# Kernel optimization log

Measured on AMD Instinct MI355X. Metric: run time of the kernel, lower is better.

## Reference

```python
import jax, jax.numpy as jnp
import numpy as np

B, C, R, E, H = 32, 64, 63, 256, 4
D = E // H  # head dim = 64


def setup_inputs() -> dict:
    key = jax.random.key(0)
    ks = jax.random.split(key, 8)
    s = 0.02
    return {
        "x": jax.random.normal(ks[0], (B, C, R, E), jnp.float32),
        "real_cols": jax.random.randint(ks[1], (B,), 0, C),
        "cls_token": jax.random.normal(ks[2], (E,), jnp.float32),
        "w_in": (jax.random.normal(ks[3], (3 * E, E), jnp.float32) * s),
        "b_in": jnp.zeros((3 * E,), jnp.float32),
        "w_out": (jax.random.normal(ks[4], (E, E), jnp.float32) * s),
        "b_out": jnp.zeros((E,), jnp.float32),
        "ln_g": jnp.ones((E,), jnp.float32),
        "ln_b": jnp.zeros((E,), jnp.float32),
        "w1": (jax.random.normal(ks[5], (E, E), jnp.float32) * s),
        "b1": jnp.zeros((E,), jnp.float32),
        "w2": (jax.random.normal(ks[6], (E, E), jnp.float32) * s),
        "b2": jnp.zeros((E,), jnp.float32),
    }


def reference(x, real_cols, cls_token, w_in, b_in, w_out, b_out, ln_g, ln_b, w1, b1, w2, b2):
    # x: (B, C, R, E); one fused batched MHA+LN+FFN over all (B, C) columns.
    Bq, Cq, Rq, Eq = x.shape
    S = Rq + 1
    cls = jnp.broadcast_to(cls_token, (Bq, Cq, 1, Eq))
    seq = jnp.concatenate([cls, x], axis=2)  # (B,C,S,E)

    # torch MultiheadAttention in-projection: x @ W^T + b, packed q|k|v
    qkv = seq @ w_in.T + b_in  # (B,C,S,3E)
    q, k, v = jnp.split(qkv, 3, axis=-1)
    q = q.reshape(Bq, Cq, S, H, D)
    k = k.reshape(Bq, Cq, S, H, D)
    v = v.reshape(Bq, Cq, S, H, D)

    scale = 1.0 / jnp.sqrt(jnp.asarray(D, x.dtype))
    scores = jnp.einsum('bcqhd,bckhd->bchqk', q, k) * scale  # (B,C,H,S,S)
    attn = jax.nn.softmax(scores, axis=-1)
    ctx = jnp.einsum('bchqk,bckhd->bcqhd', attn, v).reshape(Bq, Cq, S, Eq)
    attn_out = ctx @ w_out.T + b_out  # (B,C,S,E)

    # LayerNorm (biased variance, eps=1e-5 as in torch)
    mu = attn_out.mean(axis=-1, keepdims=True)
    var = ((attn_out - mu) ** 2).mean(axis=-1, keepdims=True)
    ln = (attn_out - mu) / jnp.sqrt(var + 1e-5) * ln_g + ln_b

    ffn = jax.nn.relu(ln @ w1.T + b1) @ w2.T + b2
    out = ln + ffn  # (B,C,S,E)

    rep = out[:, :, 0, :]  # rep_mode == 'cls'

    # columns >= real_cols[b] are zero-padded, matching the original loop
    mask = jnp.arange(Cq)[None, :] < real_cols[:, None]
    return jnp.where(mask[..., None], rep, jnp.zeros((), x.dtype))
```

## Files before the change

### kernel.cpp

```cpp
#include <hip/hip_runtime.h>
#include <hip/hip_bf16.h>
#include <cstdint>

typedef unsigned short u16;
typedef uint32_t u32;

#define Bq 32
#define Cq 64
#define Rq 63
#define NB 4

__device__ __forceinline__ float bflo(u32 u){ return __uint_as_float(u << 16); }
__device__ __forceinline__ float bfhi(u32 u){ return __uint_as_float(u & 0xffff0000u); }
__device__ __forceinline__ float bf1(u16 u){ return __uint_as_float(((u32)u) << 16); }
__device__ __forceinline__ u16 tobf(float f){ __hip_bfloat16 h = __float2bfloat16(f); return *(u16*)&h; }

__device__ __forceinline__ bool dtype_is_bf16(const void* ln_g){
    return *(const u32*)ln_g == 0x3F803F80u;
}
__device__ __forceinline__ float ldin(const void* p, int i, bool bf){
    return bf ? bf1(((const u16*)p)[i]) : ((const float*)p)[i];
}


__global__ __launch_bounds__(256) void prep_kernel(
    const void* __restrict__ cls, const void* __restrict__ w_in,
    const void* __restrict__ b_in, const void* __restrict__ w_out,
    const void* __restrict__ w1, const void* __restrict__ w2,
    const void* __restrict__ ln_g_flag,
    float* __restrict__ uf, float* __restrict__ sbf,
    u16* __restrict__ wvT, u16* __restrict__ woT,
    u16* __restrict__ w1T, u16* __restrict__ w2T)
{
    const bool bf = dtype_is_bf16(ln_g_flag);
    const int tid = threadIdx.x;
    const int blk = blockIdx.x;
    __shared__ float q0[256];
    __shared__ __align__(16) float clsf[256];

    if (blk < 256) {
        const int e = blk, j = tid;
        const int dsti = ((j >> 3) * 256 + e) * 8 + (j & 7);
        wvT[dsti] = tobf(ldin(w_in, (512 + e) * 256 + j, bf));
        woT[dsti] = tobf(ldin(w_out, e * 256 + j, bf));
        w1T[dsti] = tobf(ldin(w1,    e * 256 + j, bf));
        w2T[dsti] = tobf(ldin(w2,    e * 256 + j, bf));
        return;
    }

    const int h = blk - 256;
    clsf[tid] = ldin(cls, tid, bf);
    __syncthreads();

    {
        float acc = ldin(b_in, tid, bf);
        if (bf) {
            const u16* wr = (const u16*)w_in + tid * 256;
            #pragma unroll 8
            for (int j8 = 0; j8 < 32; ++j8) {
                uint4 w = *(const uint4*)(wr + j8 * 8);
                const float* c = &clsf[j8 * 8];
                acc += bflo(w.x) * c[0] + bfhi(w.x) * c[1]
                     + bflo(w.y) * c[2] + bfhi(w.y) * c[3]
                     + bflo(w.z) * c[4] + bfhi(w.z) * c[5]
                     + bflo(w.w) * c[6] + bfhi(w.w) * c[7];
            }
        } else {
            const float4* wr = (const float4*)((const float*)w_in + tid * 256);
            #pragma unroll 8
            for (int j4 = 0; j4 < 64; ++j4) {
                float4 w = wr[j4];
                float4 c = *(const float4*)&clsf[j4 * 4];
                acc += w.x * c.x + w.y * c.y + w.z * c.z + w.w * c.w;
            }
        }
        q0[tid] = acc;
    }
    __syncthreads();

    {
        float ua = 0.f;
        #pragma unroll 8
        for (int d = 0; d < 64; ++d)
            ua += q0[h * 64 + d] * ldin(w_in, (256 + h * 64 + d) * 256 + tid, bf);
        uf[h * 256 + tid] = ua * 0.125f;
    }
    if (tid < 64) {
        float p = q0[h * 64 + tid] * ldin(b_in, 256 + h * 64 + tid, bf);
        #pragma unroll
        for (int off = 32; off; off >>= 1) p += __shfl_xor(p, off);
        if (tid == 0) sbf[h] = p * 0.125f;
    }
}

template<int NBv>
__device__ __forceinline__ void dotN(const u16* __restrict__ wp,
                                     const float* __restrict__ vecs, int vstride,
                                     float* __restrict__ acc)
{
    #pragma unroll 2
    for (int j8 = 0; j8 < 32; ++j8) {
        uint4 w = *(const uint4*)(wp + j8 * 2048);
        float w0 = bflo(w.x), w1_ = bfhi(w.x), w2_ = bflo(w.y), w3 = bfhi(w.y);
        float w4 = bflo(w.z), w5 = bfhi(w.z), w6 = bflo(w.w), w7 = bfhi(w.w);
        #pragma unroll
        for (int i = 0; i < NBv; ++i) {
            const float* v = vecs + i * vstride + j8 * 8;
            float4 a = *(const float4*)v;
            float4 bq = *(const float4*)(v + 4);
            acc[i] += w0 * a.x + w1_ * a.y + w2_ * a.z + w3 * a.w
                    + w4 * bq.x + w5 * bq.y + w6 * bq.z + w7 * bq.w;
        }
    }
}

__global__ __launch_bounds__(256) void fused_kernel(
    const void* __restrict__ x, const int* __restrict__ real_cols,
    const void* __restrict__ cls,
    const void* __restrict__ b_in, const void* __restrict__ b_out,
    const void* __restrict__ ln_g, const void* __restrict__ ln_b,
    const void* __restrict__ b1p, const void* __restrict__ b2p,
    const float* __restrict__ uf, const float* __restrict__ sbf,
    const u16* __restrict__ wvT, const u16* __restrict__ woT,
    const u16* __restrict__ w1T, const u16* __restrict__ w2T,
    void* __restrict__ out)
{
    const bool bf = dtype_is_bf16(ln_g);
    const int tid = threadIdx.x;
    const int b = blockIdx.x >> 4;
    const int g = blockIdx.x & 15;
    const int c0 = g * NB;
    const int rc = real_cols[b];
    const int e = tid;

    if (c0 >= rc) {
        #pragma unroll
        for (int i = 0; i < NB; ++i) {
            size_t oi = (((size_t)b << 6) + c0 + i) * 256 + e;
            if (bf) ((u16*)out)[oi] = 0; else ((float*)out)[oi] = 0.f;
        }
        return;
    }

    __shared__ __align__(16) u16   lds_seq[64 * 260];
    __shared__ __align__(16) float lds_u[1024];
    __shared__ __align__(16) float lds_a[256];
    __shared__ float lds_sb[4];
    __shared__ __align__(16) float lds_s[NB * 1024];
    __shared__ __align__(16) float lds_ctx[NB * 256];
    __shared__ __align__(16) float lds_ln[NB * 256];
    __shared__ __align__(16) float lds_h1[NB * 256];
    __shared__ float lds_redA[4 * NB];
    __shared__ float lds_redB[4 * NB];

    #pragma unroll
    for (int q = 0; q < 4; ++q) lds_u[q * 256 + tid] = uf[q * 256 + tid];
    if (tid < 4) lds_sb[tid] = sbf[tid];

    if (bf) {
        if (tid < 32) {
            uint4 val = *(const uint4*)((const u16*)cls + tid * 8);
            uint2* p = (uint2*)&lds_seq[tid * 8];
            p[0] = make_uint2(val.x, val.y);
            p[1] = make_uint2(val.z, val.w);
        }
    } else {
        if (tid < 64) {
            float4 v = *(const float4*)((const float*)cls + tid * 4);
            u32 lo = ((u32)tobf(v.y) << 16) | tobf(v.x);
            u32 hi = ((u32)tobf(v.w) << 16) | tobf(v.z);
            *(uint2*)&lds_seq[tid * 4] = make_uint2(lo, hi);
        }
    }

    const int hw = tid >> 6, lt = tid & 63;

    for (int i = 0; i < NB; ++i) {
        const int c = c0 + i;
        const int bc = (b << 6) + c;
        const bool act = (c < rc);

        if (act) {
            if (bf) {
                const u16* xr = (const u16*)x + (size_t)bc * (Rq * 256);
                #pragma unroll
                for (int k = 0; k < 8; ++k) {
                    int idx = k * 256 + tid;
                    if (idx < 2016) {
                        uint4 val = *(const uint4*)(xr + idx * 8);
                        int tt = (idx >> 5) + 1;
                        int col = (idx & 31) * 8;
                        uint2* p = (uint2*)&lds_seq[tt * 260 + col];
                        p[0] = make_uint2(val.x, val.y);
                        p[1] = make_uint2(val.z, val.w);
                    }
                }
            } else {
                const float* xr = (const float*)x + (size_t)bc * (Rq * 256);
                #pragma unroll
                for (int k = 0; k < 16; ++k) {
                    int idx = k * 256 + tid;
                    if (idx < 4032) {
                        float4 v = *(const float4*)(xr + idx * 4);
                        int tt = (idx >> 6) + 1;
                        int col = (idx & 63) * 4;
                        u32 lo = ((u32)tobf(v.y) << 16) | tobf(v.x);
                        u32 hi = ((u32)tobf(v.w) << 16) | tobf(v.z);
                        *(uint2*)&lds_seq[tt * 260 + col] = make_uint2(lo, hi);
                    }
                }
            }
        }
        __syncthreads();

        if (act) {
            float sc = lds_sb[hw];
            {
                const u16* srow = &lds_seq[lt * 260];
                const float* uh = &lds_u[hw * 256];
                #pragma unroll 8
                for (int j = 0; j < 256; j += 4) {
                    uint2 pv = *(const uint2*)&srow[j];
                    float4 uv = *(const float4*)&uh[j];
                    sc += bflo(pv.x) * uv.x + bfhi(pv.x) * uv.y
                        + bflo(pv.y) * uv.z + bfhi(pv.y) * uv.w;
                }
            }
            float m = sc;
            #pragma unroll
            for (int off = 32; off; off >>= 1) m = fmaxf(m, __shfl_xor(m, off));
            float ev = __expf(sc - m);
            float sum = ev;
            #pragma unroll
            for (int off = 32; off; off >>= 1) sum += __shfl_xor(sum, off);
            lds_a[lt * 4 + hw] = ev / sum;
        }
        __syncthreads();

        {
            float* sp = &lds_s[i * 1024];
            if (act) {
                float s0 = 0.f, s1 = 0.f, s2 = 0.f, s3 = 0.f;
                #pragma unroll 4
                for (int tt = 0; tt < 64; ++tt) {
                    float v = bf1(lds_seq[tt * 260 + tid]);
                    float4 at = *(const float4*)&lds_a[tt * 4];
                    s0 += at.x * v; s1 += at.y * v; s2 += at.z * v; s3 += at.w * v;
                }
                sp[tid]       = s0;
                sp[256 + tid] = s1;
                sp[512 + tid] = s2;
                sp[768 + tid] = s3;
            } else {
                sp[tid] = 0.f; sp[256 + tid] = 0.f;
                sp[512 + tid] = 0.f; sp[768 + tid] = 0.f;
            }
        }
        __syncthreads();
    }

    const int h = tid >> 6;

    {
        float acc[NB];
        float bv = ldin(b_in, 512 + e, bf);
        #pragma unroll
        for (int i = 0; i < NB; ++i) acc[i] = bv;
        dotN<NB>(wvT + e * 8, &lds_s[h * 256], 1024, acc);
        #pragma unroll
        for (int i = 0; i < NB; ++i) lds_ctx[i * 256 + e] = acc[i];
    }
    __syncthreads();

    float ao[NB];
    {
        float bo = ldin(b_out, e, bf);
        #pragma unroll
        for (int i = 0; i < NB; ++i) ao[i] = bo;
        dotN<NB>(woT + e * 8, lds_ctx, 256, ao);
    }

    const int lane = tid & 63, wv = tid >> 6;
    float mu[NB];
    {
        float r[NB];
        #pragma unroll
        for (int i = 0; i < NB; ++i) r[i] = ao[i];
        #pragma unroll
        for (int off = 32; off; off >>= 1) {
            #pragma unroll
            for (int i = 0; i < NB; ++i) r[i] += __shfl_xor(r[i], off);
        }
        if (lane == 0) {
            #pragma unroll
            for (int i = 0; i < NB; ++i) lds_redA[wv * NB + i] = r[i];
        }
    }
    __syncthreads();
    #pragma unroll
    for (int i = 0; i < NB; ++i)
        mu[i] = (lds_redA[i] + lds_redA[NB + i] + lds_redA[2 * NB + i] + lds_redA[3 * NB + i]) * (1.f / 256.f);

    float lnv[NB];
    {
        float r[NB];
        #pragma unroll
        for (int i = 0; i < NB; ++i) { float d = ao[i] - mu[i]; r[i] = d * d; }
        #pragma unroll
        for (int off = 32; off; off >>= 1) {
            #pragma unroll
            for (int i = 0; i < NB; ++i) r[i] += __shfl_xor(r[i], off);
        }
        if (lane == 0) {
            #pragma unroll
            for (int i = 0; i < NB; ++i) lds_redB[wv * NB + i] = r[i];
        }
    }
    __syncthreads();
    {
        float gg = ldin(ln_g, e, bf), bb = ldin(ln_b, e, bf);
        #pragma unroll
        for (int i = 0; i < NB; ++i) {
            float var = (lds_redB[i] + lds_redB[NB + i] + lds_redB[2 * NB + i] + lds_redB[3 * NB + i]) * (1.f / 256.f);
            lnv[i] = (ao[i] - mu[i]) * rsqrtf(var + 1e-5f) * gg + bb;
            lds_ln[i * 256 + e] = lnv[i];
        }
    }
    __syncthreads();

    {
        float h1[NB];
        float bv = ldin(b1p, e, bf);
        #pragma unroll
        for (int i = 0; i < NB; ++i) h1[i] = bv;
        dotN<NB>(w1T + e * 8, lds_ln, 256, h1);
        #pragma unroll
        for (int i = 0; i < NB; ++i) lds_h1[i * 256 + e] = fmaxf(h1[i], 0.f);
    }
    __syncthreads();

    {
        float o[NB];
        float bv = ldin(b2p, e, bf);
        #pragma unroll
        for (int i = 0; i < NB; ++i) o[i] = lnv[i] + bv;
        dotN<NB>(w2T + e * 8, lds_h1, 256, o);
        #pragma unroll
        for (int i = 0; i < NB; ++i) {
            int c = c0 + i;
            float val = (c < rc) ? o[i] : 0.f;
            size_t oi = (((size_t)b << 6) + c) * 256 + e;
            if (bf) ((u16*)out)[oi] = tobf(val); else ((float*)out)[oi] = val;
        }
    }
}

extern "C" void kernel_launch(void* const* d_in, const int* in_sizes, int n_in,
                              void* d_out, int out_size, void* d_ws, size_t ws_size,
                              hipStream_t stream) {
    const void* x     = d_in[0];
    const int* rcols  = (const int*)d_in[1];
    const void* cls   = d_in[2];
    const void* w_in  = d_in[3];
    const void* b_in  = d_in[4];
    const void* w_out = d_in[5];
    const void* b_out = d_in[6];
    const void* ln_g  = d_in[7];
    const void* ln_b  = d_in[8];
    const void* w1    = d_in[9];
    const void* b1    = d_in[10];
    const void* w2    = d_in[11];
    const void* b2    = d_in[12];

    char* ws = (char*)d_ws;
    float* uf  = (float*)(ws);
    float* sbf = (float*)(ws + 4096);
    u16* wvT = (u16*)(ws + 4608);
    u16* woT = (u16*)(ws + 4608 + 131072);
    u16* w1T = (u16*)(ws + 4608 + 2 * 131072);
    u16* w2T = (u16*)(ws + 4608 + 3 * 131072);

    prep_kernel<<<260, 256, 0, stream>>>(cls, w_in, b_in, w_out, w1, w2, ln_g,
                                         uf, sbf, wvT, woT, w1T, w2T);
    fused_kernel<<<Bq * (Cq / NB), 256, 0, stream>>>(x, rcols, cls,
                                                     b_in, b_out, ln_g, ln_b,
                                                     b1, b2, uf, sbf,
                                                     wvT, woT, w1T, w2T, d_out);
}
```

Baseline: 260.2 us.

## Use MFMA bf16 matrix cores for per-column projection layers and prefetch next column

Replaces the scalar fp32 dot-product loops for the V, output, and FFN projections with 16x16x32 bf16 MFMA instructions. The prep kernel lays weights out in MFMA-fragment order, and the intermediate activations are stored as bf16 in a single reused shared buffer. It also prefetches the next column's input into registers while the current column's attention runs. The cost is extra rounding to bf16 of intermediate activations, and only 4 of the 16 MFMA rows carry real data.

```diff
diff --git a/kernel.cpp b/kernel.cpp
--- a/kernel.cpp
+++ b/kernel.cpp
@@ -9,6 +9,10 @@
 #define Cq 64
 #define Rq 63
 #define NB 4
+#define SEQ_ST 264
+
+typedef __attribute__((ext_vector_type(8))) short bf16x8;
+typedef __attribute__((ext_vector_type(4))) float f32x4;
 
 __device__ __forceinline__ float bflo(u32 u){ return __uint_as_float(u << 16); }
 __device__ __forceinline__ float bfhi(u32 u){ return __uint_as_float(u & 0xffff0000u); }
@@ -40,7 +44,7 @@
 
     if (blk < 256) {
         const int e = blk, j = tid;
-        const int dsti = ((j >> 3) * 256 + e) * 8 + (j & 7);
+        const int dsti = (((e >> 4) * 512) + ((j >> 5) * 64) + (((j >> 3) & 3) * 16) + (e & 15)) * 8 + (j & 7);
         wvT[dsti] = tobf(ldin(w_in, (512 + e) * 256 + j, bf));
         woT[dsti] = tobf(ldin(w_out, e * 256 + j, bf));
         w1T[dsti] = tobf(ldin(w1,    e * 256 + j, bf));
@@ -93,23 +97,23 @@
     }
 }
 
-template<int NBv>
-__device__ __forceinline__ void dotN(const u16* __restrict__ wp,
-                                     const float* __restrict__ vecs, int vstride,
-                                     float* __restrict__ acc)
+__device__ __forceinline__ void mfma_layer4(const u16* __restrict__ wbase,
+                                            const u16* __restrict__ Abase,
+                                            int lane, int w,
+                                            f32x4 acc[4])
 {
-    #pragma unroll 2
-    for (int j8 = 0; j8 < 32; ++j8) {
-        uint4 w = *(const uint4*)(wp + j8 * 2048);
-        float w0 = bflo(w.x), w1_ = bfhi(w.x), w2_ = bflo(w.y), w3 = bfhi(w.y);
-        float w4 = bflo(w.z), w5 = bfhi(w.z), w6 = bflo(w.w), w7 = bfhi(w.w);
-        #pragma unroll
-        for (int i = 0; i < NBv; ++i) {
-            const float* v = vecs + i * vstride + j8 * 8;
-            float4 a = *(const float4*)v;
-            float4 bq = *(const float4*)(v + 4);
-            acc[i] += w0 * a.x + w1_ * a.y + w2_ * a.z + w3 * a.w
-                    + w4 * bq.x + w5 * bq.y + w6 * bq.z + w7 * bq.w;
+    bf16x8 af[8];
+    const u16* ap = Abase + (lane & 15) * SEQ_ST + (lane >> 4) * 8;
+    #pragma unroll
+    for (int ks = 0; ks < 8; ++ks)
+        af[ks] = *(const bf16x8*)(ap + ks * 32);
+    const u16* wp0 = wbase + (((w * 4) * 512 + lane) << 3);
+    #pragma unroll
+    for (int ks = 0; ks < 8; ++ks) {
+        #pragma unroll
+        for (int nt = 0; nt < 4; ++nt) {
+            bf16x8 bfr = *(const bf16x8*)(wp0 + ((nt * 512 + ks * 64) << 3));
+            acc[nt] = __builtin_amdgcn_mfma_f32_16x16x32_bf16(af[ks], bfr, acc[nt], 0, 0, 0);
         }
     }
 }
@@ -142,16 +146,18 @@
         return;
     }
 
-    __shared__ __align__(16) u16   lds_seq[64 * 260];
-    __shared__ __align__(16) float lds_u[1024];
-    __shared__ __align__(16) float lds_a[256];
-    __shared__ float lds_sb[4];
-    __shared__ __align__(16) float lds_s[NB * 1024];
-    __shared__ __align__(16) float lds_ctx[NB * 256];
-    __shared__ __align__(16) float lds_ln[NB * 256];
-    __shared__ __align__(16) float lds_h1[NB * 256];
-    __shared__ float lds_redA[4 * NB];
-    __shared__ float lds_redB[4 * NB];
+    __shared__ __align__(16) char smem[53840];
+    u16*   seq    = (u16*)smem;
+    u16*   ctxB   = (u16*)smem;
+    float* aoF    = (float*)(smem + 8448);
+    u16*   lnB    = (u16*)(smem + 12544);
+    u16*   h1B    = (u16*)(smem + 20992);
+    float* lds_u  = (float*)(smem + 33792);
+    float* lds_a  = (float*)(smem + 37888);
+    float* lds_sb = (float*)(smem + 38912);
+    u16*   sB     = (u16*)(smem + 38928);
+    float* redA   = (float*)(smem + 53712);
+    float* redB   = (float*)(smem + 53776);
 
     #pragma unroll
     for (int q = 0; q < 4; ++q) lds_u[q * 256 + tid] = uf[q * 256 + tid];
@@ -160,70 +166,89 @@
     if (bf) {
         if (tid < 32) {
             uint4 val = *(const uint4*)((const u16*)cls + tid * 8);
-            uint2* p = (uint2*)&lds_seq[tid * 8];
-            p[0] = make_uint2(val.x, val.y);
-            p[1] = make_uint2(val.z, val.w);
+            *(uint4*)&seq[tid * 8] = val;
         }
     } else {
         if (tid < 64) {
             float4 v = *(const float4*)((const float*)cls + tid * 4);
             u32 lo = ((u32)tobf(v.y) << 16) | tobf(v.x);
             u32 hi = ((u32)tobf(v.w) << 16) | tobf(v.z);
-            *(uint2*)&lds_seq[tid * 4] = make_uint2(lo, hi);
-        }
-    }
-
-    const int hw = tid >> 6, lt = tid & 63;
+            *(uint2*)&seq[tid * 4] = make_uint2(lo, hi);
+        }
+    }
+
+    const int w = tid >> 6, lane = tid & 63;
+
+    uint4 stg[8];
+    float4 stgf[16];
+    auto load_col = [&](int c) {
+        int bc2 = (b << 6) + c;
+        if (bf) {
+            const u16* xr = (const u16*)x + (size_t)bc2 * (Rq * 256);
+            #pragma unroll
+            for (int k = 0; k < 8; ++k) {
+                int idx = k * 256 + tid;
+                if (idx < 2016) stg[k] = *(const uint4*)(xr + idx * 8);
+            }
+        } else {
+            const float* xr = (const float*)x + (size_t)bc2 * (Rq * 256);
+            #pragma unroll
+            for (int k = 0; k < 16; ++k) {
+                int idx = k * 256 + tid;
+                if (idx < 4032) stgf[k] = *(const float4*)(xr + idx * 4);
+            }
+        }
+    };
+    auto write_col = [&]() {
+        if (bf) {
+            #pragma unroll
+            for (int k = 0; k < 8; ++k) {
+                int idx = k * 256 + tid;
+                if (idx < 2016) {
+                    int tt = (idx >> 5) + 1, col = (idx & 31) * 8;
+                    *(uint4*)&seq[tt * SEQ_ST + col] = stg[k];
+                }
+            }
+        } else {
+            #pragma unroll
+            for (int k = 0; k < 16; ++k) {
+                int idx = k * 256 + tid;
+                if (idx < 4032) {
+                    float4 v = stgf[k];
+                    int tt = (idx >> 6) + 1, col = (idx & 63) * 4;
+                    u32 lo = ((u32)tobf(v.y) << 16) | tobf(v.x);
+                    u32 hi = ((u32)tobf(v.w) << 16) | tobf(v.z);
+                    *(uint2*)&seq[tt * SEQ_ST + col] = make_uint2(lo, hi);
+                }
+            }
+        }
+    };
+
+    load_col(c0);
 
     for (int i = 0; i < NB; ++i) {
         const int c = c0 + i;
-        const int bc = (b << 6) + c;
         const bool act = (c < rc);
 
+        if (act) write_col();
+        __syncthreads();
+
+        if (i + 1 < NB && c0 + i + 1 < rc) load_col(c0 + i + 1);
+
         if (act) {
-            if (bf) {
-                const u16* xr = (const u16*)x + (size_t)bc * (Rq * 256);
-                #pragma unroll
-                for (int k = 0; k < 8; ++k) {
-                    int idx = k * 256 + tid;
-                    if (idx < 2016) {
-                        uint4 val = *(const uint4*)(xr + idx * 8);
-                        int tt = (idx >> 5) + 1;
-                        int col = (idx & 31) * 8;
-                        uint2* p = (uint2*)&lds_seq[tt * 260 + col];
-                        p[0] = make_uint2(val.x, val.y);
-                        p[1] = make_uint2(val.z, val.w);
-                    }
-                }
-            } else {
-                const float* xr = (const float*)x + (size_t)bc * (Rq * 256);
-                #pragma unroll
-                for (int k = 0; k < 16; ++k) {
-                    int idx = k * 256 + tid;
-                    if (idx < 4032) {
-                        float4 v = *(const float4*)(xr + idx * 4);
-                        int tt = (idx >> 6) + 1;
-                        int col = (idx & 63) * 4;
-                        u32 lo = ((u32)tobf(v.y) << 16) | tobf(v.x);
-                        u32 hi = ((u32)tobf(v.w) << 16) | tobf(v.z);
-                        *(uint2*)&lds_seq[tt * 260 + col] = make_uint2(lo, hi);
-                    }
-                }
-            }
-        }
-        __syncthreads();
-
-        if (act) {
-            float sc = lds_sb[hw];
+            float sc = lds_sb[w];
             {
-                const u16* srow = &lds_seq[lt * 260];
-                const float* uh = &lds_u[hw * 256];
-                #pragma unroll 8
-                for (int j = 0; j < 256; j += 4) {
-                    uint2 pv = *(const uint2*)&srow[j];
-                    float4 uv = *(const float4*)&uh[j];
-                    sc += bflo(pv.x) * uv.x + bfhi(pv.x) * uv.y
-                        + bflo(pv.y) * uv.z + bfhi(pv.y) * uv.w;
+                const u16* srow = &seq[lane * SEQ_ST];
+                const float* uh = &lds_u[w * 256];
+                #pragma unroll 4
+                for (int j = 0; j < 256; j += 8) {
+                    uint4 pv = *(const uint4*)(srow + j);
+                    float4 u0 = *(const float4*)(uh + j);
+                    float4 u1 = *(const float4*)(uh + j + 4);
+                    sc += bflo(pv.x) * u0.x + bfhi(pv.x) * u0.y
+                        + bflo(pv.y) * u0.z + bfhi(pv.y) * u0.w
+                        + bflo(pv.z) * u1.x + bfhi(pv.z) * u1.y
+                        + bflo(pv.w) * u1.z + bfhi(pv.w) * u1.w;
                 }
             }
             float m = sc;
@@ -233,54 +258,69 @@
             float sum = ev;
             #pragma unroll
             for (int off = 32; off; off >>= 1) sum += __shfl_xor(sum, off);
-            lds_a[lt * 4 + hw] = ev / sum;
+            lds_a[lane * 4 + w] = ev / sum;
         }
         __syncthreads();
 
-        {
-            float* sp = &lds_s[i * 1024];
-            if (act) {
-                float s0 = 0.f, s1 = 0.f, s2 = 0.f, s3 = 0.f;
-                #pragma unroll 4
-                for (int tt = 0; tt < 64; ++tt) {
-                    float v = bf1(lds_seq[tt * 260 + tid]);
-                    float4 at = *(const float4*)&lds_a[tt * 4];
-                    s0 += at.x * v; s1 += at.y * v; s2 += at.z * v; s3 += at.w * v;
-                }
-                sp[tid]       = s0;
-                sp[256 + tid] = s1;
-                sp[512 + tid] = s2;
-                sp[768 + tid] = s3;
-            } else {
-                sp[tid] = 0.f; sp[256 + tid] = 0.f;
-                sp[512 + tid] = 0.f; sp[768 + tid] = 0.f;
-            }
+        if (act) {
+            float s0 = 0.f, s1 = 0.f, s2 = 0.f, s3 = 0.f;
+            #pragma unroll 4
+            for (int tt = 0; tt < 64; ++tt) {
+                float v = bf1(seq[tt * SEQ_ST + tid]);
+                float4 at = *(const float4*)&lds_a[tt * 4];
+                s0 += at.x * v; s1 += at.y * v; s2 += at.z * v; s3 += at.w * v;
+            }
+            sB[(0  + i) * SEQ_ST + tid] = tobf(s0);
+            sB[(4  + i) * SEQ_ST + tid] = tobf(s1);
+            sB[(8  + i) * SEQ_ST + tid] = tobf(s2);
+            sB[(12 + i) * SEQ_ST + tid] = tobf(s3);
+        } else {
+            sB[(0  + i) * SEQ_ST + tid] = 0;
+            sB[(4  + i) * SEQ_ST + tid] = 0;
+            sB[(8  + i) * SEQ_ST + tid] = 0;
+            sB[(12 + i) * SEQ_ST + tid] = 0;
         }
         __syncthreads();
     }
 
-    const int h = tid >> 6;
-
-    {
-        float acc[NB];
-        float bv = ldin(b_in, 512 + e, bf);
-        #pragma unroll
-        for (int i = 0; i < NB; ++i) acc[i] = bv;
-        dotN<NB>(wvT + e * 8, &lds_s[h * 256], 1024, acc);
-        #pragma unroll
-        for (int i = 0; i < NB; ++i) lds_ctx[i * 256 + e] = acc[i];
+    f32x4 acc[4];
+
+    #pragma unroll
+    for (int nt = 0; nt < 4; ++nt) {
+        float bv = ldin(b_in, 512 + w * 64 + nt * 16 + (lane & 15), bf);
+        acc[nt] = (f32x4){bv, bv, bv, bv};
+    }
+    mfma_layer4(wvT, sB + w * 4 * SEQ_ST, lane, w, acc);
+    if (lane < 16) {
+        #pragma unroll
+        for (int nt = 0; nt < 4; ++nt) {
+            int n = w * 64 + nt * 16 + lane;
+            #pragma unroll
+            for (int r = 0; r < 4; ++r) ctxB[r * SEQ_ST + n] = tobf(acc[nt][r]);
+        }
+    }
+    __syncthreads();
+
+    #pragma unroll
+    for (int nt = 0; nt < 4; ++nt) {
+        float bv = ldin(b_out, w * 64 + nt * 16 + (lane & 15), bf);
+        acc[nt] = (f32x4){bv, bv, bv, bv};
+    }
+    mfma_layer4(woT, ctxB, lane, w, acc);
+    if (lane < 16) {
+        #pragma unroll
+        for (int nt = 0; nt < 4; ++nt) {
+            int n = w * 64 + nt * 16 + lane;
+            #pragma unroll
+            for (int r = 0; r < 4; ++r) aoF[r * 256 + n] = acc[nt][r];
+        }
     }
     __syncthreads();
 
     float ao[NB];
-    {
-        float bo = ldin(b_out, e, bf);
-        #pragma unroll
-        for (int i = 0; i < NB; ++i) ao[i] = bo;
-        dotN<NB>(woT + e * 8, lds_ctx, 256, ao);
-    }
-
-    const int lane = tid & 63, wv = tid >> 6;
+    #pragma unroll
+    for (int i = 0; i < NB; ++i) ao[i] = aoF[i * 256 + e];
+
     float mu[NB];
     {
         float r[NB];
@@ -293,13 +333,13 @@
         }
         if (lane == 0) {
             #pragma unroll
-            for (int i = 0; i < NB; ++i) lds_redA[wv * NB + i] = r[i];
+            for (int i = 0; i < NB; ++i) redA[w * NB + i] = r[i];
         }
     }
     __syncthreads();
     #pragma unroll
     for (int i = 0; i < NB; ++i)
-        mu[i] = (lds_redA[i] + lds_redA[NB + i] + lds_redA[2 * NB + i] + lds_redA[3 * NB + i]) * (1.f / 256.f);
+        mu[i] = (redA[i] + redA[NB + i] + redA[2 * NB + i] + redA[3 * NB + i]) * (1.f / 256.f);
 
     float lnv[NB];
     {
@@ -313,7 +353,7 @@
         }
         if (lane == 0) {
             #pragma unroll
-            for (int i = 0; i < NB; ++i) lds_redB[wv * NB + i] = r[i];
+            for (int i = 0; i < NB; ++i) redB[w * NB + i] = r[i];
         }
     }
     __syncthreads();
@@ -321,37 +361,52 @@
         float gg = ldin(ln_g, e, bf), bb = ldin(ln_b, e, bf);
         #pragma unroll
         for (int i = 0; i < NB; ++i) {
-            float var = (lds_redB[i] + lds_redB[NB + i] + lds_redB[2 * NB + i] + lds_redB[3 * NB + i]) * (1.f / 256.f);
+            float var = (redB[i] + redB[NB + i] + redB[2 * NB + i] + redB[3 * NB + i]) * (1.f / 256.f);
             lnv[i] = (ao[i] - mu[i]) * rsqrtf(var + 1e-5f) * gg + bb;
-            lds_ln[i * 256 + e] = lnv[i];
-        }
-    }
-    __syncthreads();
-
-    {
-        float h1[NB];
-        float bv = ldin(b1p, e, bf);
-        #pragma unroll
-        for (int i = 0; i < NB; ++i) h1[i] = bv;
-        dotN<NB>(w1T + e * 8, lds_ln, 256, h1);
-        #pragma unroll
-        for (int i = 0; i < NB; ++i) lds_h1[i * 256 + e] = fmaxf(h1[i], 0.f);
-    }
-    __syncthreads();
-
-    {
-        float o[NB];
-        float bv = ldin(b2p, e, bf);
-        #pragma unroll
-        for (int i = 0; i < NB; ++i) o[i] = lnv[i] + bv;
-        dotN<NB>(w2T + e * 8, lds_h1, 256, o);
-        #pragma unroll
-        for (int i = 0; i < NB; ++i) {
-            int c = c0 + i;
-            float val = (c < rc) ? o[i] : 0.f;
-            size_t oi = (((size_t)b << 6) + c) * 256 + e;
-            if (bf) ((u16*)out)[oi] = tobf(val); else ((float*)out)[oi] = val;
-        }
+            lnB[i * SEQ_ST + e] = tobf(lnv[i]);
+        }
+    }
+    __syncthreads();
+
+    #pragma unroll
+    for (int nt = 0; nt < 4; ++nt) {
+        float bv = ldin(b1p, w * 64 + nt * 16 + (lane & 15), bf);
+        acc[nt] = (f32x4){bv, bv, bv, bv};
+    }
+    mfma_layer4(w1T, lnB, lane, w, acc);
+    if (lane < 16) {
+        #pragma unroll
+        for (int nt = 0; nt < 4; ++nt) {
+            int n = w * 64 + nt * 16 + lane;
+            #pragma unroll
+            for (int r = 0; r < 4; ++r) h1B[r * SEQ_ST + n] = tobf(fmaxf(acc[nt][r], 0.f));
+        }
+    }
+    __syncthreads();
+
+    #pragma unroll
+    for (int nt = 0; nt < 4; ++nt) {
+        float bv = ldin(b2p, w * 64 + nt * 16 + (lane & 15), bf);
+        acc[nt] = (f32x4){bv, bv, bv, bv};
+    }
+    mfma_layer4(w2T, h1B, lane, w, acc);
+    float* oF = aoF;
+    if (lane < 16) {
+        #pragma unroll
+        for (int nt = 0; nt < 4; ++nt) {
+            int n = w * 64 + nt * 16 + lane;
+            #pragma unroll
+            for (int r = 0; r < 4; ++r) oF[r * 256 + n] = acc[nt][r];
+        }
+    }
+    __syncthreads();
+
+    #pragma unroll
+    for (int i = 0; i < NB; ++i) {
+        int c = c0 + i;
+        float val = (c < rc) ? (oF[i * 256 + e] + lnv[i]) : 0.f;
+        size_t oi = (((size_t)b << 6) + c) * 256 + e;
+        if (bf) ((u16*)out)[oi] = tobf(val); else ((float*)out)[oi] = val;
     }
 }
 
```

After: 233.7 us (median of 2 runs). 10.2% less time.
